# Performance work log

Measured on AMD Instinct MI355X. Metric: run time of the kernel, lower is better.

## Reference

```python
import jax, jax.numpy as jnp
import numpy as np

EPS = 1e-5  # nn.BatchNorm1d default eps


def setup_inputs() -> dict:
    key = jax.random.key(0)
    ks = jax.random.split(key, 8)
    N_NODES, N_EDGES = 50000, 800000
    D_NODE, D_EDGE, HID, NCLS = 128, 64, 256, 8
    D_IN = D_EDGE + 2 * D_NODE  # 320
    return {
        "n_feats": jax.random.normal(ks[0], (N_NODES, D_NODE), dtype=jnp.float32),
        "edge_feats": jax.random.normal(ks[1], (N_EDGES, D_EDGE), dtype=jnp.float32),
        "src_idx": jax.random.randint(ks[2], (N_EDGES,), 0, N_NODES, dtype=jnp.int64),
        "dst_idx": jax.random.randint(ks[3], (N_EDGES,), 0, N_NODES, dtype=jnp.int64),
        "W1": jax.random.normal(ks[4], (HID, D_IN), dtype=jnp.float32) * (1.0 / np.sqrt(D_IN)),
        "b1": jnp.zeros((HID,), dtype=jnp.float32),
        "gamma": jnp.ones((HID,), dtype=jnp.float32),
        "beta": jnp.zeros((HID,), dtype=jnp.float32),
        "W2": jax.random.normal(ks[5], (NCLS, HID), dtype=jnp.float32) * (1.0 / np.sqrt(HID)),
        "b2": jnp.zeros((NCLS,), dtype=jnp.float32),
    }


def reference(n_feats, edge_feats, src_idx, dst_idx, W1, b1, gamma, beta, W2, b2):
    # gather-concat: [E, d_edge + 2*d_node]
    h = jnp.concatenate([edge_feats, n_feats[src_idx], n_feats[dst_idx]], axis=1)
    # Linear 1
    z = jnp.einsum("ei,hi->eh", h, W1) + b1
    # BatchNorm1d in training mode: batch mean / biased variance over edges
    mu = jnp.mean(z, axis=0)
    var = jnp.mean(jnp.square(z - mu), axis=0)
    zn = (z - mu) * jax.lax.rsqrt(var + EPS) * gamma + beta
    # Linear 2 + LogSoftmax(dim=1)
    logits = jnp.einsum("eh,ch->ec", zn, W2) + b2
    return jax.nn.log_softmax(logits, axis=1)
```

## Files before the change

### kernel.cpp

```cpp
#include <hip/hip_runtime.h>
#include <hip/hip_bf16.h>


#define N_EDGES 800000
#define N_NODES 50000

typedef __attribute__((ext_vector_type(8))) short short8;
typedef __attribute__((ext_vector_type(4))) float f32x4;

#define WS_SUM   0
#define WS_SQ    16384
#define WS_CVEC  32768
#define WS_FLAG  32832
#define WS_MBIG  33280
#define WS_MB    43520
#define WS_MF    45568
#define WS_W1B   55808
#define WS_PS    262144
#define WS_PD    2097152
#define WS_NFB   4194304
#define WS_FAST_NEED (4u << 20)
#define WS_BIG_NEED  16994304u

__device__ __forceinline__ ushort f2bf(float f) {
    union { float f; unsigned int u; } x; x.f = f;
    unsigned int r = x.u + 0x7FFFu + ((x.u >> 16) & 1u);
    return (ushort)(r >> 16);
}
__device__ __forceinline__ short8 cvt8(const float* __restrict__ p) {
    short8 r;
    #pragma unroll
    for (int i = 0; i < 8; i++) r[i] = (short)f2bf(p[i]);
    return r;
}
__device__ __forceinline__ short8 cvtpair(uint4 a, uint4 b) {
    unsigned int v[8] = {a.x, a.y, a.z, a.w, b.x, b.y, b.z, b.w};
    short8 r;
    #pragma unroll
    for (int i = 0; i < 8; i++) {
        unsigned int u = v[i];
        unsigned int rr = u + 0x7FFFu + ((u >> 16) & 1u);
        r[i] = (short)(rr >> 16);
    }
    return r;
}

__device__ __forceinline__ int aidx(int s, int r, int c) {
    return ((s * 64 + r) * 4 + (c ^ ((r >> 1) & 3))) * 8;
}

__global__ void detect_kernel(const int* __restrict__ src,
                              const int* __restrict__ dst, int* flag) {
    int t = threadIdx.x;
    int v = src[2 * t + 1] | dst[2 * t + 1];
    #pragma unroll
    for (int o = 32; o >= 1; o >>= 1) v |= __shfl_xor(v, o);
    if (t == 0) *flag = (v == 0) ? 1 : 0;
}

__global__ __launch_bounds__(256) void prep_kernel(const float* __restrict__ W1,
                                                   ushort* __restrict__ W1b) {
    const int i = (blockIdx.x * 256 + threadIdx.x) * 4;
    const float4 v = *(const float4*)(W1 + i);
    ushort4 o;
    o.x = f2bf(v.x); o.y = f2bf(v.y); o.z = f2bf(v.z); o.w = f2bf(v.w);
    *(ushort4*)(W1b + i) = o;
}

__global__ __launch_bounds__(256) void prep_all_kernel(
    const float* __restrict__ nf, const float* __restrict__ W1,
    const int* __restrict__ src, const int* __restrict__ dst,
    ushort* __restrict__ nfb, ushort* __restrict__ W1b,
    float* __restrict__ zreg, int* __restrict__ flag)
{
    const int t = threadIdx.x;
    const int b = blockIdx.x;
    if (b < 3125) {
        const long i = (long)b * 2048 + t * 8;
        const float4 v0 = *(const float4*)(nf + i);
        const float4 v1 = *(const float4*)(nf + i + 4);
        short8 o;
        o[0] = (short)f2bf(v0.x); o[1] = (short)f2bf(v0.y);
        o[2] = (short)f2bf(v0.z); o[3] = (short)f2bf(v0.w);
        o[4] = (short)f2bf(v1.x); o[5] = (short)f2bf(v1.y);
        o[6] = (short)f2bf(v1.z); o[7] = (short)f2bf(v1.w);
        *(short8*)(nfb + i) = o;
    } else if (b < 3205) {
        const int i = (b - 3125) * 1024 + t * 4;
        const float4 v = *(const float4*)(W1 + i);
        ushort4 o;
        o.x = f2bf(v.x); o.y = f2bf(v.y); o.z = f2bf(v.z); o.w = f2bf(v.w);
        *(ushort4*)(W1b + i) = o;
    } else {
        for (int i = t; i < 8320; i += 256) zreg[i] = 0.f;
        __syncthreads();
        if (t < 64) {
            int v = src[2 * t + 1] | dst[2 * t + 1];
            #pragma unroll
            for (int o = 32; o >= 1; o >>= 1) v |= __shfl_xor(v, o);
            if (t == 0) *flag = (v == 0) ? 1 : 0;
        }
    }
}

template <bool NFB>
__global__ __launch_bounds__(256) void gemm1_stats_kernel(
    const float* __restrict__ nf, const ushort* __restrict__ nfb,
    const float* __restrict__ ef,
    const int* __restrict__ src, const int* __restrict__ dst,
    const ushort* __restrict__ W1b, const int* __restrict__ flag,
    float* __restrict__ g_sum, float* __restrict__ g_sq)
{
    __shared__ ushort a_lds[10 * 64 * 32];

    const int t    = threadIdx.x;
    const int lane = t & 63;
    const int wave = t >> 6;
    const int quad = lane >> 4;
    const int l15  = lane & 15;

    const int wide = *flag;
    const int r = t >> 2, chunk = t & 3;
    const long e  = (long)blockIdx.x * 64 + r;
    const int si = src[e << wide], di = dst[e << wide];
    const float* pe = ef + e * 64 + chunk * 8;

    uint4 pe0[2], pe1[2];
    pe0[0] = *(const uint4*)pe;        pe0[1] = *(const uint4*)(pe + 4);
    pe1[0] = *(const uint4*)(pe + 32); pe1[1] = *(const uint4*)(pe + 36);

    const ushort* wbase = W1b + (wave * 64 + l15) * 320 + quad * 8;
    short8 bpre[2][4];
    #pragma unroll
    for (int in = 0; in < 4; in++)
        bpre[0][in] = *(const short8*)(wbase + in * 16 * 320);
    #pragma unroll
    for (int in = 0; in < 4; in++)
        bpre[1][in] = *(const short8*)(wbase + in * 16 * 320 + 32);

    if constexpr (NFB) {
        const ushort* psb = nfb + (long)si * 128 + chunk * 8;
        const ushort* pdb = nfb + (long)di * 128 + chunk * 8;
        short8 g[8];
        #pragma unroll
        for (int i = 0; i < 4; i++) g[i]     = *(const short8*)(psb + i * 32);
        #pragma unroll
        for (int i = 0; i < 4; i++) g[4 + i] = *(const short8*)(pdb + i * 32);
        *(short8*)&a_lds[aidx(0, r, chunk)] = cvtpair(pe0[0], pe0[1]);
        *(short8*)&a_lds[aidx(1, r, chunk)] = cvtpair(pe1[0], pe1[1]);
        #pragma unroll
        for (int i = 0; i < 8; i++)
            *(short8*)&a_lds[aidx(2 + i, r, chunk)] = g[i];
    } else {
        const float* ps = nf + (long)si * 128 + chunk * 8;
        const float* pd = nf + (long)di * 128 + chunk * 8;
        uint4 pn[16];
        #pragma unroll
        for (int i = 0; i < 4; i++) {
            pn[i * 2]     = *(const uint4*)(ps + i * 32);
            pn[i * 2 + 1] = *(const uint4*)(ps + i * 32 + 4);
        }
        #pragma unroll
        for (int i = 0; i < 4; i++) {
            pn[8 + i * 2]     = *(const uint4*)(pd + i * 32);
            pn[8 + i * 2 + 1] = *(const uint4*)(pd + i * 32 + 4);
        }
        *(short8*)&a_lds[aidx(0, r, chunk)] = cvtpair(pe0[0], pe0[1]);
        *(short8*)&a_lds[aidx(1, r, chunk)] = cvtpair(pe1[0], pe1[1]);
        #pragma unroll
        for (int i = 0; i < 8; i++)
            *(short8*)&a_lds[aidx(2 + i, r, chunk)] =
                cvtpair(pn[i * 2], pn[i * 2 + 1]);
    }
    __syncthreads();

    f32x4 acc[4][4];
    #pragma unroll
    for (int a = 0; a < 4; a++)
        #pragma unroll
        for (int b = 0; b < 4; b++) acc[a][b] = (f32x4){0.f, 0.f, 0.f, 0.f};

    short8 acur[4], anext[4];
    #pragma unroll
    for (int mb = 0; mb < 4; mb++)
        acur[mb] = *(const short8*)&a_lds[aidx(0, mb * 16 + l15, quad)];

    #pragma unroll
    for (int ks = 0; ks < 10; ks++) {
        short8 bcur[4];
        #pragma unroll
        for (int in = 0; in < 4; in++) bcur[in] = bpre[ks & 1][in];
        if (ks < 8) {
            #pragma unroll
            for (int in = 0; in < 4; in++)
                bpre[ks & 1][in] =
                    *(const short8*)(wbase + in * 16 * 320 + (ks + 2) * 32);
        }
        if (ks < 9) {
            #pragma unroll
            for (int mb = 0; mb < 4; mb++)
                anext[mb] = *(const short8*)
                    &a_lds[aidx(ks + 1, mb * 16 + l15, quad)];
        }
        __builtin_amdgcn_s_setprio(1);
        #pragma unroll
        for (int mb = 0; mb < 4; mb++)
            #pragma unroll
            for (int in = 0; in < 4; in++)
                acc[mb][in] = __builtin_amdgcn_mfma_f32_16x16x32_bf16(
                    acur[mb], bcur[in], acc[mb][in], 0, 0, 0);
        __builtin_amdgcn_s_setprio(0);
        #pragma unroll
        for (int mb = 0; mb < 4; mb++) acur[mb] = anext[mb];
    }

    const int slot = blockIdx.x & 15;
    #pragma unroll
    for (int in = 0; in < 4; in++) {
        const int col = wave * 64 + in * 16 + l15;
        float s = 0.f, q = 0.f;
        #pragma unroll
        for (int mb = 0; mb < 4; mb++)
            #pragma unroll
            for (int j = 0; j < 4; j++) {
                float v = acc[mb][in][j];
                s += v; q += v * v;
            }
        s += __shfl_xor(s, 16); s += __shfl_xor(s, 32);
        q += __shfl_xor(q, 16); q += __shfl_xor(q, 32);
        if (quad == 0) {
            atomicAdd(&g_sum[slot * 256 + col], s);
            atomicAdd(&g_sq[slot * 256 + col], q);
        }
    }
}

__global__ __launch_bounds__(256) void fold_kernel(
    const float* __restrict__ gamma, const float* __restrict__ beta,
    const float* __restrict__ W1, const float* __restrict__ b1,
    const float* __restrict__ W2, const float* __restrict__ b2,
    const float* __restrict__ g_sum, const float* __restrict__ g_sq,
    ushort* __restrict__ Mbig, ushort* __restrict__ Mb,
    float* __restrict__ Mf, float* __restrict__ Cvec)
{
    __shared__ float a_sh[256][8];
    __shared__ float red[8];
    __shared__ float mk_sh[64][8];
    const int t = threadIdx.x;

    float ssum = 0.f, ssq = 0.f;
    #pragma unroll
    for (int s = 0; s < 16; s++) {
        ssum += g_sum[s * 256 + t];
        ssq  += g_sq[s * 256 + t];
    }
    const float invE   = 1.0f / (float)N_EDGES;
    const float mu_acc = ssum * invE;
    float var = ssq * invE - mu_acc * mu_acc;
    var = fmaxf(var, 0.f);
    const float b1v = b1[t];
    const float mu  = mu_acc + b1v;
    const float g   = gamma[t] * rsqrtf(var + 1e-5f);
    const float sh  = b1v * g + beta[t] - mu * g;

    if (t < 8) red[t] = 0.f;
    ((float*)mk_sh)[t] = 0.f;
    ((float*)mk_sh)[t + 256] = 0.f;
    __syncthreads();
    #pragma unroll
    for (int c = 0; c < 8; c++) {
        const float w = W2[c * 256 + t];
        a_sh[t][c] = w * g;
        if (blockIdx.x == 0) atomicAdd(&red[c], w * sh);
    }
    __syncthreads();

    const int k  = blockIdx.x * 64 + (t & 63);
    const int q4 = t >> 6;
    float m[8] = {0.f, 0.f, 0.f, 0.f, 0.f, 0.f, 0.f, 0.f};
    for (int hh = q4 * 64; hh < q4 * 64 + 64; hh++) {
        const float w1 = W1[hh * 320 + k];
        #pragma unroll
        for (int c = 0; c < 8; c++) m[c] += a_sh[hh][c] * w1;
    }
    #pragma unroll
    for (int c = 0; c < 8; c++) atomicAdd(&mk_sh[t & 63][c], m[c]);
    __syncthreads();

    if (t < 64) {
        const int kk = blockIdx.x * 64 + t;
        #pragma unroll
        for (int c = 0; c < 8; c++) {
            const float mv = mk_sh[t][c];
            Mf[c * 320 + kk]   = mv;
            Mbig[c * 320 + kk] = f2bf(mv);
            if (kk < 64) Mb[c * 64 + kk] = f2bf(mv);
        }
        #pragma unroll
        for (int c = 8; c < 16; c++) {
            Mbig[c * 320 + kk] = 0;
            if (kk < 64) Mb[c * 64 + kk] = 0;
        }
    }
    if (blockIdx.x == 0) {
        if (t < 8)       Cvec[t] = b2[t] + red[t];
        else if (t < 16) Cvec[t] = 0.f;
    }
}

__global__ __launch_bounds__(256) void fold_nodeproj_kernel(
    const float* __restrict__ gamma, const float* __restrict__ beta,
    const float* __restrict__ W1, const float* __restrict__ b1,
    const float* __restrict__ W2, const float* __restrict__ b2,
    const float* __restrict__ g_sum, const float* __restrict__ g_sq,
    const float* __restrict__ nf, ushort* __restrict__ Mb,
    float* __restrict__ Cvec, float* __restrict__ Ps, float* __restrict__ Pd)
{
    __shared__ float a_sh[256][8];
    __shared__ float red[8];
    __shared__ float Ms[8][128];
    __shared__ float Md[8][128];
    const int t = threadIdx.x;

    float ssum = 0.f, ssq = 0.f;
    #pragma unroll
    for (int s = 0; s < 16; s++) {
        ssum += g_sum[s * 256 + t];
        ssq  += g_sq[s * 256 + t];
    }
    const float invE   = 1.0f / (float)N_EDGES;
    const float mu_acc = ssum * invE;
    float var = ssq * invE - mu_acc * mu_acc;
    var = fmaxf(var, 0.f);
    const float b1v = b1[t];
    const float mu  = mu_acc + b1v;
    const float g   = gamma[t] * rsqrtf(var + 1e-5f);
    const float sh  = b1v * g + beta[t] - mu * g;

    if (t < 8) red[t] = 0.f;
    __syncthreads();
    #pragma unroll
    for (int c = 0; c < 8; c++) {
        const float w = W2[c * 256 + t];
        a_sh[t][c] = w * g;
        if (blockIdx.x == 0) atomicAdd(&red[c], w * sh);
    }
    __syncthreads();

    float m[8] = {0.f, 0.f, 0.f, 0.f, 0.f, 0.f, 0.f, 0.f};
    for (int hh = 0; hh < 256; hh++) {
        const float w1 = W1[hh * 320 + 64 + t];
        #pragma unroll
        for (int c = 0; c < 8; c++) m[c] += a_sh[hh][c] * w1;
    }
    #pragma unroll
    for (int c = 0; c < 8; c++) {
        if (t < 128) Ms[c][t] = m[c];
        else         Md[c][t - 128] = m[c];
    }
    if (blockIdx.x == 0) {
        if (t < 64) {
            float mm[8] = {0.f, 0.f, 0.f, 0.f, 0.f, 0.f, 0.f, 0.f};
            for (int hh = 0; hh < 256; hh++) {
                const float w1 = W1[hh * 320 + t];
                #pragma unroll
                for (int c = 0; c < 8; c++) mm[c] += a_sh[hh][c] * w1;
            }
            #pragma unroll
            for (int c = 0; c < 8; c++)  Mb[c * 64 + t] = f2bf(mm[c]);
            #pragma unroll
            for (int c = 8; c < 16; c++) Mb[c * 64 + t] = 0;
        }
        if (t < 8)       Cvec[t] = b2[t] + red[t];
        else if (t < 16) Cvec[t] = 0.f;
    }
    __syncthreads();

    const int n = blockIdx.x * 256 + t;
    if (n >= N_NODES) return;
    float as[8] = {0,0,0,0,0,0,0,0}, ad[8] = {0,0,0,0,0,0,0,0};
    for (int k = 0; k < 128; k += 4) {
        const float4 v = *(const float4*)(nf + (long)n * 128 + k);
        #pragma unroll
        for (int c = 0; c < 8; c++) {
            const float4 ms = *(const float4*)&Ms[c][k];
            const float4 md = *(const float4*)&Md[c][k];
            as[c] += v.x * ms.x + v.y * ms.y + v.z * ms.z + v.w * ms.w;
            ad[c] += v.x * md.x + v.y * md.y + v.z * md.z + v.w * md.w;
        }
    }
    #pragma unroll
    for (int c = 0; c < 8; c++) {
        Ps[n * 8 + c] = as[c];
        Pd[n * 8 + c] = ad[c];
    }
}

__global__ __launch_bounds__(256) void nodeproj_kernel(
    const float* __restrict__ nf, const float* __restrict__ Mf,
    float* __restrict__ Ps, float* __restrict__ Pd)
{
    __shared__ float Ms[8][128];
    __shared__ float Md[8][128];
    const int t = threadIdx.x;
    #pragma unroll
    for (int i = 0; i < 4; i++) {
        const int f = t + i * 256;
        Ms[f >> 7][f & 127] = Mf[(f >> 7) * 320 + 64  + (f & 127)];
        Md[f >> 7][f & 127] = Mf[(f >> 7) * 320 + 192 + (f & 127)];
    }
    __syncthreads();
    const int n = blockIdx.x * 256 + t;
    if (n >= N_NODES) return;
    float as[8] = {0,0,0,0,0,0,0,0}, ad[8] = {0,0,0,0,0,0,0,0};
    for (int k = 0; k < 128; k += 4) {
        const float4 v = *(const float4*)(nf + (long)n * 128 + k);
        #pragma unroll
        for (int c = 0; c < 8; c++) {
            const float4 ms = *(const float4*)&Ms[c][k];
            const float4 md = *(const float4*)&Md[c][k];
            as[c] += v.x * ms.x + v.y * ms.y + v.z * ms.z + v.w * ms.w;
            ad[c] += v.x * md.x + v.y * md.y + v.z * md.z + v.w * md.w;
        }
    }
    #pragma unroll
    for (int c = 0; c < 8; c++) {
        Ps[n * 8 + c] = as[c];
        Pd[n * 8 + c] = ad[c];
    }
}

__global__ __launch_bounds__(256) void edge_out_kernel(
    const float* __restrict__ ef, const int* __restrict__ src,
    const int* __restrict__ dst, const int* __restrict__ flag,
    const ushort* __restrict__ Mb, const float* __restrict__ Ps,
    const float* __restrict__ Pd, const float* __restrict__ Cvec,
    float* __restrict__ out)
{
    __shared__ float pv_sh[4][64][9];
    const int t    = threadIdx.x;
    const int lane = t & 63;
    const int wave = t >> 6;
    const int quad = lane >> 4;
    const int l15  = lane & 15;
    const int wide = *flag;
    const long eb  = (long)blockIdx.x * 256 + wave * 64;

    const long ei = (eb + lane) << wide;
    const int sidx = src[ei], didx = dst[ei];
    const float4 s0 = *(const float4*)(Ps + sidx * 8);
    const float4 s1 = *(const float4*)(Ps + sidx * 8 + 4);
    const float4 d0 = *(const float4*)(Pd + didx * 8);
    const float4 d1 = *(const float4*)(Pd + didx * 8 + 4);

    uint4 ea[4][2], eb4[4][2];
    #pragma unroll
    for (int mb = 0; mb < 4; mb++)
        #pragma unroll
        for (int ks = 0; ks < 2; ks++) {
            const float* p = ef + (eb + mb * 16 + l15) * 64 + ks * 32 + quad * 8;
            ea[mb][ks]  = *(const uint4*)p;
            eb4[mb][ks] = *(const uint4*)(p + 4);
        }

    pv_sh[wave][lane][0] = s0.x + d0.x;
    pv_sh[wave][lane][1] = s0.y + d0.y;
    pv_sh[wave][lane][2] = s0.z + d0.z;
    pv_sh[wave][lane][3] = s0.w + d0.w;
    pv_sh[wave][lane][4] = s1.x + d1.x;
    pv_sh[wave][lane][5] = s1.y + d1.y;
    pv_sh[wave][lane][6] = s1.z + d1.z;
    pv_sh[wave][lane][7] = s1.w + d1.w;

    f32x4 acc[4];
    #pragma unroll
    for (int mb = 0; mb < 4; mb++) acc[mb] = (f32x4){0.f, 0.f, 0.f, 0.f};

    const ushort* bbase = Mb + l15 * 64 + quad * 8;
    #pragma unroll
    for (int ks = 0; ks < 2; ks++) {
        short8 bfr = *(const short8*)(bbase + ks * 32);
        #pragma unroll
        for (int mb = 0; mb < 4; mb++)
            acc[mb] = __builtin_amdgcn_mfma_f32_16x16x32_bf16(
                cvtpair(ea[mb][ks], eb4[mb][ks]), bfr, acc[mb], 0, 0, 0);
    }

    const float bv = Cvec[l15];
    #pragma unroll
    for (int mb = 0; mb < 4; mb++) {
        #pragma unroll
        for (int j = 0; j < 4; j++) {
            const int er = mb * 16 + quad * 4 + j;
            const float pv = (l15 < 8) ? pv_sh[wave][er][l15] : 0.f;
            float x = acc[mb][j] + bv + pv;
            float m = x;
            m = fmaxf(m, __shfl_xor(m, 1));
            m = fmaxf(m, __shfl_xor(m, 2));
            m = fmaxf(m, __shfl_xor(m, 4));
            float sx = __expf(x - m);
            sx += __shfl_xor(sx, 1);
            sx += __shfl_xor(sx, 2);
            sx += __shfl_xor(sx, 4);
            const float o = x - m - __logf(sx);
            if (l15 < 8) out[(eb + er) * 8 + l15] = o;
        }
    }
}

__global__ __launch_bounds__(256) void out_kernel(
    const float* __restrict__ nf, const float* __restrict__ ef,
    const int* __restrict__ src, const int* __restrict__ dst,
    const int* __restrict__ flag, const ushort* __restrict__ M,
    const float* __restrict__ Cvec, float* __restrict__ out)
{
    const int t    = threadIdx.x;
    const int lane = t & 63;
    const int wave = t >> 6;
    const int quad = lane >> 4;
    const int l15  = lane & 15;
    const int wide = *flag;
    const long eb  = (long)blockIdx.x * 256 + wave * 64;

    const float* pe[4]; const float* ps[4]; const float* pd[4];
    #pragma unroll
    for (int mb = 0; mb < 4; mb++) {
        const long e  = eb + mb * 16 + l15;
        const int si = src[e << wide], di = dst[e << wide];
        pe[mb] = ef + e * 64;
        ps[mb] = nf + (long)si * 128;
        pd[mb] = nf + (long)di * 128;
    }
    f32x4 acc[4];
    #pragma unroll
    for (int mb = 0; mb < 4; mb++) acc[mb] = (f32x4){0.f, 0.f, 0.f, 0.f};
    const ushort* bbase = M + l15 * 320 + quad * 8;
    #pragma unroll
    for (int ks = 0; ks < 10; ks++) {
        const int k0 = ks * 32;
        short8 bfr = *(const short8*)(bbase + k0);
        const int koff = k0 + quad * 8;
        #pragma unroll
        for (int mb = 0; mb < 4; mb++) {
            const float* p = (ks < 2) ? (pe[mb] + koff)
                           : (ks < 6) ? (ps[mb] + (koff - 64))
                                      : (pd[mb] + (koff - 192));
            acc[mb] = __builtin_amdgcn_mfma_f32_16x16x32_bf16(
                cvt8(p), bfr, acc[mb], 0, 0, 0);
        }
    }
    const float bv = Cvec[l15];
    #pragma unroll
    for (int mb = 0; mb < 4; mb++)
        #pragma unroll
        for (int j = 0; j < 4; j++) {
            float x = acc[mb][j] + bv;
            float m = x;
            m = fmaxf(m, __shfl_xor(m, 1));
            m = fmaxf(m, __shfl_xor(m, 2));
            m = fmaxf(m, __shfl_xor(m, 4));
            float sx = __expf(x - m);
            sx += __shfl_xor(sx, 1);
            sx += __shfl_xor(sx, 2);
            sx += __shfl_xor(sx, 4);
            const float o = x - m - __logf(sx);
            if (l15 < 8)
                out[(eb + mb * 16 + quad * 4 + j) * 8 + l15] = o;
        }
}

extern "C" void kernel_launch(void* const* d_in, const int* in_sizes, int n_in,
                              void* d_out, int out_size, void* d_ws, size_t ws_size,
                              hipStream_t stream) {
    const float* nf    = (const float*)d_in[0];
    const float* ef    = (const float*)d_in[1];
    const int*   src   = (const int*)d_in[2];
    const int*   dst   = (const int*)d_in[3];
    const float* W1    = (const float*)d_in[4];
    const float* b1    = (const float*)d_in[5];
    const float* gamma = (const float*)d_in[6];
    const float* beta  = (const float*)d_in[7];
    const float* W2    = (const float*)d_in[8];
    const float* b2    = (const float*)d_in[9];

    char*   ws    = (char*)d_ws;
    float*  g_sum = (float*)(ws + WS_SUM);
    float*  g_sq  = (float*)(ws + WS_SQ);
    float*  Cvec  = (float*)(ws + WS_CVEC);
    int*    flag  = (int*)(ws + WS_FLAG);
    ushort* Mbig  = (ushort*)(ws + WS_MBIG);
    ushort* Mb    = (ushort*)(ws + WS_MB);
    float*  Mf    = (float*)(ws + WS_MF);
    ushort* W1b   = (ushort*)(ws + WS_W1B);
    float*  Ps    = (float*)(ws + WS_PS);
    float*  Pd    = (float*)(ws + WS_PD);
    ushort* nfb   = (ushort*)(ws + WS_NFB);
    float*  out   = (float*)d_out;

    const bool fast = ws_size >= (size_t)WS_FAST_NEED;
    const bool big  = ws_size >= (size_t)WS_BIG_NEED;

    if (big) {
        prep_all_kernel<<<3206, 256, 0, stream>>>(nf, W1, src, dst, nfb, W1b,
                                                  (float*)ws, flag);
        gemm1_stats_kernel<true><<<N_EDGES / 64, 256, 0, stream>>>(
            nf, nfb, ef, src, dst, W1b, flag, g_sum, g_sq);
        fold_nodeproj_kernel<<<(N_NODES + 255) / 256, 256, 0, stream>>>(
            gamma, beta, W1, b1, W2, b2, g_sum, g_sq, nf, Mb, Cvec, Ps, Pd);
        edge_out_kernel<<<N_EDGES / 256, 256, 0, stream>>>(ef, src, dst, flag,
                                                           Mb, Ps, Pd, Cvec, out);
    } else {
        hipMemsetAsync(ws, 0, 33280, stream);
        detect_kernel<<<1, 64, 0, stream>>>(src, dst, flag);
        prep_kernel<<<80, 256, 0, stream>>>(W1, W1b);
        gemm1_stats_kernel<false><<<N_EDGES / 64, 256, 0, stream>>>(
            nf, nfb, ef, src, dst, W1b, flag, g_sum, g_sq);
        fold_kernel<<<5, 256, 0, stream>>>(gamma, beta, W1, b1, W2, b2,
                                           g_sum, g_sq, Mbig, Mb, Mf, Cvec);
        if (fast) {
            nodeproj_kernel<<<(N_NODES + 255) / 256, 256, 0, stream>>>(nf, Mf, Ps, Pd);
            edge_out_kernel<<<N_EDGES / 256, 256, 0, stream>>>(ef, src, dst, flag,
                                                               Mb, Ps, Pd, Cvec, out);
        } else {
            out_kernel<<<N_EDGES / 256, 256, 0, stream>>>(nf, ef, src, dst, flag,
                                                          Mbig, Cvec, out);
        }
    }
}
```

Before: 623.1 us.

## Process two 64-edge tiles per block in gemm1 to reuse W1 fragments

The gemm1_stats kernel now handles 128 edges per block as two 64-row A tiles in LDS, and each W1 B-fragment loaded from global memory feeds MFMAs for both tiles. This halves the W1 traffic per edge, halves the number of blocks and the atomic stats updates. The price is doubled accumulator registers and LDS use (launch_bounds 256,2), which lowers occupancy, and the A-fragment prefetch pipelining across k-steps is dropped.

```diff
diff --git a/kernel.cpp b/kernel.cpp
--- a/kernel.cpp
+++ b/kernel.cpp
@@ -104,14 +104,14 @@
 }
 
 template <bool NFB>
-__global__ __launch_bounds__(256) void gemm1_stats_kernel(
+__global__ __launch_bounds__(256, 2) void gemm1_stats_kernel(
     const float* __restrict__ nf, const ushort* __restrict__ nfb,
     const float* __restrict__ ef,
     const int* __restrict__ src, const int* __restrict__ dst,
     const ushort* __restrict__ W1b, const int* __restrict__ flag,
     float* __restrict__ g_sum, float* __restrict__ g_sq)
 {
-    __shared__ ushort a_lds[10 * 64 * 32];
+    __shared__ ushort a_lds[20 * 64 * 32];
 
     const int t    = threadIdx.x;
     const int lane = t & 63;
@@ -120,17 +120,26 @@
     const int l15  = lane & 15;
 
     const int wide = *flag;
-    const int r = t >> 2, chunk = t & 3;
-    const long e  = (long)blockIdx.x * 64 + r;
+    const int r    = t >> 1;
+    const int half = t & 1;
+    const int tile = r >> 6;
+    const int rr   = r & 63;
+    const long e   = (long)blockIdx.x * 128 + r;
     const int si = src[e << wide], di = dst[e << wide];
-    const float* pe = ef + e * 64 + chunk * 8;
-
-    uint4 pe0[2], pe1[2];
-    pe0[0] = *(const uint4*)pe;        pe0[1] = *(const uint4*)(pe + 4);
-    pe1[0] = *(const uint4*)(pe + 32); pe1[1] = *(const uint4*)(pe + 36);
+    const float* pe = ef + e * 64;
+
+    uint4 efu[4][2];
+    #pragma unroll
+    for (int s = 0; s < 2; s++)
+        #pragma unroll
+        for (int cj = 0; cj < 2; cj++) {
+            const float* p = pe + s * 32 + (2 * half + cj) * 8;
+            efu[s * 2 + cj][0] = *(const uint4*)p;
+            efu[s * 2 + cj][1] = *(const uint4*)(p + 4);
+        }
 
     const ushort* wbase = W1b + (wave * 64 + l15) * 320 + quad * 8;
-    short8 bpre[2][4];
+    short8 bpre[3][4];
     #pragma unroll
     for (int in = 0; in < 4; in++)
         bpre[0][in] = *(const short8*)(wbase + in * 16 * 320);
@@ -139,79 +148,109 @@
         bpre[1][in] = *(const short8*)(wbase + in * 16 * 320 + 32);
 
     if constexpr (NFB) {
-        const ushort* psb = nfb + (long)si * 128 + chunk * 8;
-        const ushort* pdb = nfb + (long)di * 128 + chunk * 8;
-        short8 g[8];
-        #pragma unroll
-        for (int i = 0; i < 4; i++) g[i]     = *(const short8*)(psb + i * 32);
-        #pragma unroll
-        for (int i = 0; i < 4; i++) g[4 + i] = *(const short8*)(pdb + i * 32);
-        *(short8*)&a_lds[aidx(0, r, chunk)] = cvtpair(pe0[0], pe0[1]);
-        *(short8*)&a_lds[aidx(1, r, chunk)] = cvtpair(pe1[0], pe1[1]);
-        #pragma unroll
-        for (int i = 0; i < 8; i++)
-            *(short8*)&a_lds[aidx(2 + i, r, chunk)] = g[i];
+        const ushort* psb = nfb + (long)si * 128;
+        const ushort* pdb = nfb + (long)di * 128;
+        short8 g[16];
+        #pragma unroll
+        for (int i = 0; i < 4; i++)
+            #pragma unroll
+            for (int cj = 0; cj < 2; cj++)
+                g[i * 2 + cj] = *(const short8*)(psb + i * 32 + (2 * half + cj) * 8);
+        #pragma unroll
+        for (int i = 0; i < 4; i++)
+            #pragma unroll
+            for (int cj = 0; cj < 2; cj++)
+                g[8 + i * 2 + cj] = *(const short8*)(pdb + i * 32 + (2 * half + cj) * 8);
+        #pragma unroll
+        for (int s = 0; s < 2; s++)
+            #pragma unroll
+            for (int cj = 0; cj < 2; cj++)
+                *(short8*)&a_lds[aidx(tile * 10 + s, rr, 2 * half + cj)] =
+                    cvtpair(efu[s * 2 + cj][0], efu[s * 2 + cj][1]);
+        #pragma unroll
+        for (int i = 0; i < 4; i++)
+            #pragma unroll
+            for (int cj = 0; cj < 2; cj++) {
+                *(short8*)&a_lds[aidx(tile * 10 + 2 + i, rr, 2 * half + cj)] =
+                    g[i * 2 + cj];
+                *(short8*)&a_lds[aidx(tile * 10 + 6 + i, rr, 2 * half + cj)] =
+                    g[8 + i * 2 + cj];
+            }
     } else {
-        const float* ps = nf + (long)si * 128 + chunk * 8;
-        const float* pd = nf + (long)di * 128 + chunk * 8;
+        const float* ps = nf + (long)si * 128;
+        const float* pd = nf + (long)di * 128;
+        #pragma unroll
+        for (int s = 0; s < 2; s++)
+            #pragma unroll
+            for (int cj = 0; cj < 2; cj++)
+                *(short8*)&a_lds[aidx(tile * 10 + s, rr, 2 * half + cj)] =
+                    cvtpair(efu[s * 2 + cj][0], efu[s * 2 + cj][1]);
         uint4 pn[16];
         #pragma unroll
-        for (int i = 0; i < 4; i++) {
-            pn[i * 2]     = *(const uint4*)(ps + i * 32);
-            pn[i * 2 + 1] = *(const uint4*)(ps + i * 32 + 4);
-        }
-        #pragma unroll
-        for (int i = 0; i < 4; i++) {
-            pn[8 + i * 2]     = *(const uint4*)(pd + i * 32);
-            pn[8 + i * 2 + 1] = *(const uint4*)(pd + i * 32 + 4);
-        }
-        *(short8*)&a_lds[aidx(0, r, chunk)] = cvtpair(pe0[0], pe0[1]);
-        *(short8*)&a_lds[aidx(1, r, chunk)] = cvtpair(pe1[0], pe1[1]);
-        #pragma unroll
-        for (int i = 0; i < 8; i++)
-            *(short8*)&a_lds[aidx(2 + i, r, chunk)] =
-                cvtpair(pn[i * 2], pn[i * 2 + 1]);
-    }
-    __syncthreads();
-
-    f32x4 acc[4][4];
-    #pragma unroll
-    for (int a = 0; a < 4; a++)
-        #pragma unroll
-        for (int b = 0; b < 4; b++) acc[a][b] = (f32x4){0.f, 0.f, 0.f, 0.f};
-
-    short8 acur[4], anext[4];
-    #pragma unroll
-    for (int mb = 0; mb < 4; mb++)
-        acur[mb] = *(const short8*)&a_lds[aidx(0, mb * 16 + l15, quad)];
+        for (int i = 0; i < 4; i++)
+            #pragma unroll
+            for (int cj = 0; cj < 2; cj++) {
+                const float* p = ps + i * 32 + (2 * half + cj) * 8;
+                pn[(i * 2 + cj) * 2]     = *(const uint4*)p;
+                pn[(i * 2 + cj) * 2 + 1] = *(const uint4*)(p + 4);
+            }
+        #pragma unroll
+        for (int i = 0; i < 4; i++)
+            #pragma unroll
+            for (int cj = 0; cj < 2; cj++)
+                *(short8*)&a_lds[aidx(tile * 10 + 2 + i, rr, 2 * half + cj)] =
+                    cvtpair(pn[(i * 2 + cj) * 2], pn[(i * 2 + cj) * 2 + 1]);
+        #pragma unroll
+        for (int i = 0; i < 4; i++)
+            #pragma unroll
+            for (int cj = 0; cj < 2; cj++) {
+                const float* p = pd + i * 32 + (2 * half + cj) * 8;
+                pn[(i * 2 + cj) * 2]     = *(const uint4*)p;
+                pn[(i * 2 + cj) * 2 + 1] = *(const uint4*)(p + 4);
+            }
+        #pragma unroll
+        for (int i = 0; i < 4; i++)
+            #pragma unroll
+            for (int cj = 0; cj < 2; cj++)
+                *(short8*)&a_lds[aidx(tile * 10 + 6 + i, rr, 2 * half + cj)] =
+                    cvtpair(pn[(i * 2 + cj) * 2], pn[(i * 2 + cj) * 2 + 1]);
+    }
+    __syncthreads();
+
+    f32x4 acc[2][4][4];
+    #pragma unroll
+    for (int tl = 0; tl < 2; tl++)
+        #pragma unroll
+        for (int a = 0; a < 4; a++)
+            #pragma unroll
+            for (int b = 0; b < 4; b++)
+                acc[tl][a][b] = (f32x4){0.f, 0.f, 0.f, 0.f};
 
     #pragma unroll
     for (int ks = 0; ks < 10; ks++) {
-        short8 bcur[4];
-        #pragma unroll
-        for (int in = 0; in < 4; in++) bcur[in] = bpre[ks & 1][in];
         if (ks < 8) {
             #pragma unroll
             for (int in = 0; in < 4; in++)
-                bpre[ks & 1][in] =
+                bpre[(ks + 2) % 3][in] =
                     *(const short8*)(wbase + in * 16 * 320 + (ks + 2) * 32);
         }
-        if (ks < 9) {
+        short8 afr[2][4];
+        #pragma unroll
+        for (int tl = 0; tl < 2; tl++)
             #pragma unroll
             for (int mb = 0; mb < 4; mb++)
-                anext[mb] = *(const short8*)
-                    &a_lds[aidx(ks + 1, mb * 16 + l15, quad)];
-        }
+                afr[tl][mb] = *(const short8*)
+                    &a_lds[aidx(tl * 10 + ks, mb * 16 + l15, quad)];
         __builtin_amdgcn_s_setprio(1);
         #pragma unroll
-        for (int mb = 0; mb < 4; mb++)
-            #pragma unroll
-            for (int in = 0; in < 4; in++)
-                acc[mb][in] = __builtin_amdgcn_mfma_f32_16x16x32_bf16(
-                    acur[mb], bcur[in], acc[mb][in], 0, 0, 0);
+        for (int tl = 0; tl < 2; tl++)
+            #pragma unroll
+            for (int mb = 0; mb < 4; mb++)
+                #pragma unroll
+                for (int in = 0; in < 4; in++)
+                    acc[tl][mb][in] = __builtin_amdgcn_mfma_f32_16x16x32_bf16(
+                        afr[tl][mb], bpre[ks % 3][in], acc[tl][mb][in], 0, 0, 0);
         __builtin_amdgcn_s_setprio(0);
-        #pragma unroll
-        for (int mb = 0; mb < 4; mb++) acur[mb] = anext[mb];
     }
 
     const int slot = blockIdx.x & 15;
@@ -220,12 +259,14 @@
         const int col = wave * 64 + in * 16 + l15;
         float s = 0.f, q = 0.f;
         #pragma unroll
-        for (int mb = 0; mb < 4; mb++)
-            #pragma unroll
-            for (int j = 0; j < 4; j++) {
-                float v = acc[mb][in][j];
-                s += v; q += v * v;
-            }
+        for (int tl = 0; tl < 2; tl++)
+            #pragma unroll
+            for (int mb = 0; mb < 4; mb++)
+                #pragma unroll
+                for (int j = 0; j < 4; j++) {
+                    float v = acc[tl][mb][in][j];
+                    s += v; q += v * v;
+                }
         s += __shfl_xor(s, 16); s += __shfl_xor(s, 32);
         q += __shfl_xor(q, 16); q += __shfl_xor(q, 32);
         if (quad == 0) {
@@ -603,7 +644,7 @@
     if (big) {
         prep_all_kernel<<<3206, 256, 0, stream>>>(nf, W1, src, dst, nfb, W1b,
                                                   (float*)ws, flag);
-        gemm1_stats_kernel<true><<<N_EDGES / 64, 256, 0, stream>>>(
+        gemm1_stats_kernel<true><<<N_EDGES / 128, 256, 0, stream>>>(
             nf, nfb, ef, src, dst, W1b, flag, g_sum, g_sq);
         fold_nodeproj_kernel<<<(N_NODES + 255) / 256, 256, 0, stream>>>(
             gamma, beta, W1, b1, W2, b2, g_sum, g_sq, nf, Mb, Cvec, Ps, Pd);
@@ -613,7 +654,7 @@
         hipMemsetAsync(ws, 0, 33280, stream);
         detect_kernel<<<1, 64, 0, stream>>>(src, dst, flag);
         prep_kernel<<<80, 256, 0, stream>>>(W1, W1b);
-        gemm1_stats_kernel<false><<<N_EDGES / 64, 256, 0, stream>>>(
+        gemm1_stats_kernel<false><<<N_EDGES / 128, 256, 0, stream>>>(
             nf, nfb, ef, src, dst, W1b, flag, g_sum, g_sq);
         fold_kernel<<<5, 256, 0, stream>>>(gamma, beta, W1, b1, W2, b2,
                                            g_sum, g_sq, Mbig, Mb, Mf, Cvec);
```

Measured after the change: 548.9 us. 1.14x faster.
